# Optimization experiments

Hardware: AMD Instinct MI355X
Metric: run time of the kernel (lower is better)

The kernel has to match this reference:

```python
import jax, jax.numpy as jnp
import numpy as np

T, B, D, L = 512, 64, 1024, 1024  # seq_len, batch, input_dim, latent_dim


def setup_inputs() -> dict:
    key = jax.random.key(0)
    ks = jax.random.split(key, 5)
    s = 1.0 / np.sqrt(D + L)  # fan-in scale for gate linears
    x = jax.random.normal(ks[0], (T, B, D), dtype=jnp.float32)
    Wf = jax.random.normal(ks[1], (D + L, L), dtype=jnp.float32) * s
    Wi = jax.random.normal(ks[2], (D + L, L), dtype=jnp.float32) * s
    Wo = jax.random.normal(ks[3], (D + L, L), dtype=jnp.float32) * s
    Wg = jax.random.normal(ks[4], (D + L, L), dtype=jnp.float32) * s
    z = jnp.zeros((L,), dtype=jnp.float32)
    return {"x": x, "Wf": Wf, "bf": z, "Wi": Wi, "bi": z,
            "Wo": Wo, "bo": z, "Wg": Wg, "bg": z}


def reference(x, Wf, bf, Wi, bi, Wo, bo, Wg, bg):
    # x: [T, B, D]; each gate W: [D+L, L]. Fuse the four gate GEMMs into one.
    L_ = Wf.shape[1]
    Wcat = jnp.concatenate([Wf, Wi, Wo, Wg], axis=1)       # [D+L, 4L]
    bcat = jnp.concatenate([bf, bi, bo, bg], axis=0)       # [4L]

    def step(carry, xt):
        h, c = carry                                        # [B, L] each
        z = jnp.concatenate([xt, h], axis=-1)               # [B, D+L]
        gates = z @ Wcat + bcat                             # [B, 4L]
        f = jax.nn.sigmoid(gates[:, 0 * L_:1 * L_])
        i = jax.nn.sigmoid(gates[:, 1 * L_:2 * L_])
        o = jax.nn.sigmoid(gates[:, 2 * L_:3 * L_])
        g = jnp.tanh(gates[:, 3 * L_:4 * L_])
        c_new = f * c + i * g
        h_new = o * jnp.tanh(c_new)
        return (h_new, c_new), h_new

    Bt = x.shape[1]
    h0 = jnp.zeros((Bt, L_), dtype=x.dtype)
    c0 = jnp.zeros((Bt, L_), dtype=x.dtype)
    _, hs = jax.lax.scan(step, (h0, c0), x)                 # hs: [T, B, L]
    return hs
```

## Files before the change

kernel.cpp:

```cpp
#include <hip/hip_runtime.h>
#include <hip/hip_bf16.h>
#include <cstdint>
#include <cstddef>

typedef short short8 __attribute__((ext_vector_type(8)));
typedef float f32x4 __attribute__((ext_vector_type(4)));
typedef int i32x4 __attribute__((ext_vector_type(4)));
typedef unsigned long long u64;
typedef unsigned int u32;

#define TT 512
#define BB 64
#define DD 1024
#define LL 1024

__global__ __launch_bounds__(256) void transpose_w(
    const float* __restrict__ Wf, const float* __restrict__ Wi,
    const float* __restrict__ Wo, const float* __restrict__ Wg,
    __hip_bfloat16* __restrict__ Wt) {
  __shared__ float tile[32][33];
  const int g = blockIdx.z;
  const float* W = (g == 0) ? Wf : (g == 1) ? Wi : (g == 2) ? Wo : Wg;
  const int k0 = blockIdx.x * 32, l0 = blockIdx.y * 32;
  const int c = threadIdx.x & 31, r0 = threadIdx.x >> 5;
#pragma unroll
  for (int rr = 0; rr < 4; ++rr) {
    const int kk = r0 + rr * 8;
    tile[kk][c] = W[(size_t)(k0 + kk) * LL + (l0 + c)];
  }
  __syncthreads();
#pragma unroll
  for (int rr = 0; rr < 4; ++rr) {
    const int ll = r0 + rr * 8;
    Wt[((size_t)(g * LL + l0 + ll) << 11) + (k0 + c)] = __float2bfloat16(tile[c][ll]);
  }
}

__global__ __launch_bounds__(256) void xconv(const float* __restrict__ x,
                                             __hip_bfloat16* __restrict__ xbf) {
  const size_t i = (size_t)blockIdx.x * 256 + threadIdx.x;
  const float4 v = ((const float4*)x)[i];
  union { __hip_bfloat16 b[4]; uint2 u; } o;
  o.b[0] = __float2bfloat16(v.x);
  o.b[1] = __float2bfloat16(v.y);
  o.b[2] = __float2bfloat16(v.z);
  o.b[3] = __float2bfloat16(v.w);
  ((uint2*)xbf)[i] = o.u;
}

__global__ __launch_bounds__(512, 2) void lstm_persist(
    const __hip_bfloat16* __restrict__ xbf, const __hip_bfloat16* __restrict__ Wt,
    const float* __restrict__ bfv, const float* __restrict__ biv,
    const float* __restrict__ bov, const float* __restrict__ bgv,
    float* __restrict__ out, __hip_bfloat16* __restrict__ hball,
    int* __restrict__ flags) {
  __shared__ short8 wf[4096];
  __shared__ float gw[4][16][17];
  __shared__ float gsx[2][64][17];
  __shared__ int ep;

  const int tid = threadIdx.x;
  const int lane = tid & 63, w = tid >> 6;
  const int quad = lane >> 4, hc = lane & 15;
  const bool isH = (w < 4);
  const int bt = w & 3;
  const int kp = isH ? 1 : 0;
  const int bid = blockIdx.x;
  const int l0 = bid * 4;

  if (tid == 0) ep = 0;

  const int col = ((hc >> 2) << 10) + l0 + (hc & 3);
  if (w == 0 || w == 4) {
    const __hip_bfloat16* wb = Wt + ((size_t)col << 11) + (kp << 10) + quad * 8;
#pragma unroll
    for (int j = 0; j < 32; ++j)
      wf[(kp << 11) + (j << 6) + lane] = *(const short8*)(wb + j * 32);
  }

  const int rowoff = (bt << 4) + hc;

  const int row16 = lane >> 2, lc = lane & 3;
  const int pl = l0 + lc;
  float cr = 0.f, bfr = 0.f, bir = 0.f, bor = 0.f, bgr = 0.f;
  if (isH) { bfr = bfv[pl]; bir = biv[pl]; bor = bov[pl]; bgr = bgv[pl]; }

  __syncthreads();

  auto xgemm = [&](int tt) {
    const __hip_bfloat16* za =
        xbf + ((size_t)tt << 16) + ((size_t)rowoff << 10) + quad * 8;
    f32x4 a0 = {}, a1 = {};
    short8 Af[2][8];
#pragma unroll
    for (int i = 0; i < 8; ++i) Af[0][i] = *(const short8*)(za + i * 32);
#pragma unroll
    for (int g = 0; g < 4; ++g) {
      const int cur = g & 1, nxt = cur ^ 1;
      if (g < 3) {
#pragma unroll
        for (int i = 0; i < 8; ++i)
          Af[nxt][i] = *(const short8*)(za + (g + 1) * 256 + i * 32);
      }
#pragma unroll
      for (int i = 0; i < 8; ++i) {
        const short8 bb = wf[((g << 3) + i) * 64 + lane];
        if (i & 1)
          a1 = __builtin_amdgcn_mfma_f32_16x16x32_bf16(Af[cur][i], bb, a1, 0, 0, 0);
        else
          a0 = __builtin_amdgcn_mfma_f32_16x16x32_bf16(Af[cur][i], bb, a0, 0, 0, 0);
      }
    }
    const int par = tt & 1;
#pragma unroll
    for (int r = 0; r < 4; ++r)
      gsx[par][(bt << 4) + (quad << 2) + r][hc] = a0[r] + a1[r];
  };

  if (!isH) xgemm(0);
  __syncthreads();

  for (int t = 0; t < TT; ++t) {
    if (!isH) {
      if (t + 1 < TT) xgemm(t + 1);
    } else {
      f32x4 a0 = {}, a1 = {};
      if (t > 0) {
        if (w == 0) {
          const int* fp4 = flags + (lane << 2);
          int ok = 0, spins = 0;
          while (!ok && spins < (1 << 14)) {
            i32x4 f;
            asm volatile("global_load_dwordx4 %0, %1, off sc0 sc1"
                         : "=v"(f) : "v"(fp4));
            asm volatile("s_waitcnt vmcnt(0)" ::: "memory");
            ok = __all((f[0] >= t) & (f[1] >= t) & (f[2] >= t) & (f[3] >= t));
            if (!ok) { __builtin_amdgcn_s_sleep(1); ++spins; }
          }
          __hip_atomic_store(&ep, t, __ATOMIC_RELAXED, __HIP_MEMORY_SCOPE_WORKGROUP);
        } else {
          int spins = 0;
          while (__hip_atomic_load(&ep, __ATOMIC_RELAXED,
                                   __HIP_MEMORY_SCOPE_WORKGROUP) < t) {
            if (++spins > (1 << 22)) break;
          }
        }
        asm volatile("" ::: "memory");

        const u64* hp = (const u64*)(hball + ((size_t)(t - 1) << 16)) +
                        (quad << 7) + rowoff;
        union frag { short8 s; u64 u[2]; };
        frag Ah[2][8];
#pragma unroll
        for (int i = 0; i < 8; ++i) {
          Ah[0][i].u[0] = hp[i * 512];
          Ah[0][i].u[1] = hp[i * 512 + 64];
        }
#pragma unroll
        for (int g = 0; g < 4; ++g) {
          const int cur = g & 1, nxt = cur ^ 1;
          if (g < 3) {
#pragma unroll
            for (int i = 0; i < 8; ++i) {
              Ah[nxt][i].u[0] = hp[(g + 1) * 4096 + i * 512];
              Ah[nxt][i].u[1] = hp[(g + 1) * 4096 + i * 512 + 64];
            }
          }
#pragma unroll
          for (int i = 0; i < 8; ++i) {
            const short8 bb = wf[2048 + ((g << 3) + i) * 64 + lane];
            if (i & 1)
              a1 = __builtin_amdgcn_mfma_f32_16x16x32_bf16(Ah[cur][i].s, bb, a1, 0, 0, 0);
            else
              a0 = __builtin_amdgcn_mfma_f32_16x16x32_bf16(Ah[cur][i].s, bb, a0, 0, 0, 0);
          }
        }
      }

#pragma unroll
      for (int r = 0; r < 4; ++r)
        gw[bt][(quad << 2) + r][hc] =
            a0[r] + a1[r] + gsx[t & 1][(bt << 4) + (quad << 2) + r][hc];

      const float fp = gw[bt][row16][lc] + bfr;
      const float ip = gw[bt][row16][4 + lc] + bir;
      const float op = gw[bt][row16][8 + lc] + bor;
      const float gp = gw[bt][row16][12 + lc] + bgr;
      const float fs = 1.0f / (1.0f + __expf(-fp));
      const float is = 1.0f / (1.0f + __expf(-ip));
      const float os = 1.0f / (1.0f + __expf(-op));
      const float gv = tanhf(gp);
      cr = fs * cr + is * gv;
      const float h = os * tanhf(cr);
      const int b = (bt << 4) + row16;
      out[((size_t)t << 16) + ((size_t)b << 10) + pl] = h;
      const float hn = __shfl_xor(h, 1);
      if ((lc & 1) == 0) {
        union { __hip_bfloat16 x[2]; u32 u; } hu;
        hu.x[0] = __float2bfloat16(h);
        hu.x[1] = __float2bfloat16(hn);
        u32* hwp = (u32*)(hball + ((size_t)t << 16));
        __hip_atomic_store(hwp + (bid << 7) + (b << 1) + (lc >> 1), hu.u,
                           __ATOMIC_RELAXED, __HIP_MEMORY_SCOPE_AGENT);
      }
    }

    asm volatile("s_waitcnt vmcnt(0)" ::: "memory");
    __syncthreads();
    if (tid == 0)
      __hip_atomic_store(&flags[bid], t + 1, __ATOMIC_RELAXED,
                         __HIP_MEMORY_SCOPE_AGENT);
  }
}

extern "C" void kernel_launch(void* const* d_in, const int* in_sizes, int n_in,
                              void* d_out, int out_size, void* d_ws, size_t ws_size,
                              hipStream_t stream) {
  const float* x   = (const float*)d_in[0];
  const float* Wf  = (const float*)d_in[1];
  const float* bfv = (const float*)d_in[2];
  const float* Wi  = (const float*)d_in[3];
  const float* biv = (const float*)d_in[4];
  const float* Wo  = (const float*)d_in[5];
  const float* bov = (const float*)d_in[6];
  const float* Wg  = (const float*)d_in[7];
  const float* bgv = (const float*)d_in[8];
  float* out = (float*)d_out;

  __hip_bfloat16* Wt    = (__hip_bfloat16*)d_ws;
  __hip_bfloat16* xbf   = Wt + (size_t)4096 * 2048;
  __hip_bfloat16* hball = xbf + (size_t)TT * BB * LL;
  int* flags = (int*)(hball + (size_t)TT * 65536);

  transpose_w<<<dim3(64, 32, 4), 256, 0, stream>>>(Wf, Wi, Wo, Wg, Wt);
  xconv<<<dim3((TT * BB * LL) / 4 / 256), 256, 0, stream>>>(x, xbf);
  hipMemsetAsync(flags, 0, 256 * sizeof(int), stream);

  lstm_persist<<<256, 512, 0, stream>>>(xbf, Wt, bfv, biv, bov, bgv,
                                        out, hball, flags);
}
```

Before: 4.386 ms.

## Replace per-block flag array barrier with single atomic counter grid barrier

Replaces the per-block flag array, which wave 0 polled with a vector load of all 256 flags, with a single global counter. Each block atomically increments the counter once per step, and one lane spins until it reaches t*256. The output store of h is moved after the barrier signal so it no longer delays the vmcnt wait before signalling. The risk is contention from 256 atomics on one address each step, and a tight spin with no sleep.

Result: slower. 4.572 ms (+4.2%).

```diff
diff --git a/kernel.cpp b/kernel.cpp
--- a/kernel.cpp
+++ b/kernel.cpp
@@ -5,7 +5,6 @@
 
 typedef short short8 __attribute__((ext_vector_type(8)));
 typedef float f32x4 __attribute__((ext_vector_type(4)));
-typedef int i32x4 __attribute__((ext_vector_type(4)));
 typedef unsigned long long u64;
 typedef unsigned int u32;
 
@@ -53,7 +52,7 @@
     const float* __restrict__ bfv, const float* __restrict__ biv,
     const float* __restrict__ bov, const float* __restrict__ bgv,
     float* __restrict__ out, __hip_bfloat16* __restrict__ hball,
-    int* __restrict__ flags) {
+    int* __restrict__ ctr) {
   __shared__ short8 wf[4096];
   __shared__ float gw[4][16][17];
   __shared__ float gsx[2][64][17];
@@ -121,28 +120,31 @@
   __syncthreads();
 
   for (int t = 0; t < TT; ++t) {
+    float hval = 0.f;
+    int b = 0;
+
     if (!isH) {
       if (t + 1 < TT) xgemm(t + 1);
     } else {
       f32x4 a0 = {}, a1 = {};
       if (t > 0) {
         if (w == 0) {
-          const int* fp4 = flags + (lane << 2);
-          int ok = 0, spins = 0;
-          while (!ok && spins < (1 << 14)) {
-            i32x4 f;
-            asm volatile("global_load_dwordx4 %0, %1, off sc0 sc1"
-                         : "=v"(f) : "v"(fp4));
-            asm volatile("s_waitcnt vmcnt(0)" ::: "memory");
-            ok = __all((f[0] >= t) & (f[1] >= t) & (f[2] >= t) & (f[3] >= t));
-            if (!ok) { __builtin_amdgcn_s_sleep(1); ++spins; }
-          }
-          __hip_atomic_store(&ep, t, __ATOMIC_RELAXED, __HIP_MEMORY_SCOPE_WORKGROUP);
-        } else {
+          if (lane == 0) {
+            const int want = t << 8;
+            int spins = 0;
+            while (__hip_atomic_load(ctr, __ATOMIC_RELAXED,
+                                     __HIP_MEMORY_SCOPE_AGENT) < want) {
+              if (++spins > (1 << 20)) break;
+            }
+            __hip_atomic_store(&ep, t, __ATOMIC_RELAXED,
+                               __HIP_MEMORY_SCOPE_WORKGROUP);
+          }
+        }
+        {
           int spins = 0;
           while (__hip_atomic_load(&ep, __ATOMIC_RELAXED,
                                    __HIP_MEMORY_SCOPE_WORKGROUP) < t) {
-            if (++spins > (1 << 22)) break;
+            if (++spins > (1 << 24)) break;
           }
         }
         asm volatile("" ::: "memory");
@@ -191,13 +193,13 @@
       const float os = 1.0f / (1.0f + __expf(-op));
       const float gv = tanhf(gp);
       cr = fs * cr + is * gv;
-      const float h = os * tanhf(cr);
-      const int b = (bt << 4) + row16;
-      out[((size_t)t << 16) + ((size_t)b << 10) + pl] = h;
-      const float hn = __shfl_xor(h, 1);
+      hval = os * tanhf(cr);
+      b = (bt << 4) + row16;
+
+      const float hn = __shfl_xor(hval, 1);
       if ((lc & 1) == 0) {
         union { __hip_bfloat16 x[2]; u32 u; } hu;
-        hu.x[0] = __float2bfloat16(h);
+        hu.x[0] = __float2bfloat16(hval);
         hu.x[1] = __float2bfloat16(hn);
         u32* hwp = (u32*)(hball + ((size_t)t << 16));
         __hip_atomic_store(hwp + (bid << 7) + (b << 1) + (lc >> 1), hu.u,
@@ -208,8 +210,11 @@
     asm volatile("s_waitcnt vmcnt(0)" ::: "memory");
     __syncthreads();
     if (tid == 0)
-      __hip_atomic_store(&flags[bid], t + 1, __ATOMIC_RELAXED,
-                         __HIP_MEMORY_SCOPE_AGENT);
+      __hip_atomic_fetch_add(ctr, 1, __ATOMIC_RELAXED,
+                             __HIP_MEMORY_SCOPE_AGENT);
+
+    if (isH)
+      out[((size_t)t << 16) + ((size_t)b << 10) + pl] = hval;
   }
 }
 
@@ -230,12 +235,12 @@
   __hip_bfloat16* Wt    = (__hip_bfloat16*)d_ws;
   __hip_bfloat16* xbf   = Wt + (size_t)4096 * 2048;
   __hip_bfloat16* hball = xbf + (size_t)TT * BB * LL;
-  int* flags = (int*)(hball + (size_t)TT * 65536);
+  int* ctr = (int*)(hball + (size_t)TT * 65536);
 
   transpose_w<<<dim3(64, 32, 4), 256, 0, stream>>>(Wf, Wi, Wo, Wg, Wt);
   xconv<<<dim3((TT * BB * LL) / 4 / 256), 256, 0, stream>>>(x, xbf);
-  hipMemsetAsync(flags, 0, 256 * sizeof(int), stream);
+  hipMemsetAsync(ctr, 0, 256 * sizeof(int), stream);
 
   lstm_persist<<<256, 512, 0, stream>>>(xbf, Wt, bfv, biv, bov, bgv,
-                                        out, hball, flags);
-}
+                                        out, hball, ctr);
+}
```
